# Optimization experiments

Hardware: AMD Instinct MI355X
Metric: run time of the kernel (lower is better)

## Reference

```python
import jax, jax.numpy as jnp
import numpy as np

HIDDEN = 100


def _mlp(x, w1, b1, w2, b2):
    # MLP(in, HIDDEN, output_size=out): Linear -> ReLU -> Linear
    return jnp.maximum(x @ w1 + b1, 0.0) @ w2 + b2


def _row_norm_mean(d):
    # mean_i sqrt(sum_j d_ij^2)  == torch.sqrt(einsum('ij,ij->i')).mean()
    return jnp.sqrt(jnp.einsum('ij,ij->i', d, d)).mean()


def _mismatch_1nn(mapped, target, idx):
    # torch_mapping_misclassified_1nn: cdist(mapped[idx], target), top-1 NN,
    # count non-integer distances at mismatched rows / len(idx).
    a = mapped[idx]                                     # [K, d]
    d2 = (jnp.sum(a * a, axis=1, keepdims=True)
          + jnp.sum(target * target, axis=1)[None, :]
          - 2.0 * a @ target.T)                         # [K, N]
    dist = jnp.sqrt(jnp.maximum(d2, 0.0))
    vals = jnp.min(dist, axis=1)                        # top-1 smallest value
    nn_inds = jnp.argmin(dist, axis=1)
    mismatch = (nn_inds != idx)
    count = (jnp.ceil(vals) - jnp.floor(vals)) * mismatch.astype(vals.dtype)
    return count.sum() / idx.shape[0]


def setup_inputs() -> dict:
    key = jax.random.key(0)
    ks = jax.random.split(key, 8)
    xN, yN, xd, yd, K = 25000, 25000, 100, 120, 8000
    s = 0.1
    return {
        'x_weight': jax.random.normal(ks[0], (xN, xd), jnp.float32) * s,
        'y_weight': jax.random.normal(ks[1], (yN, yd), jnp.float32) * s,
        'fx_w1': jax.random.normal(ks[2], (xd, HIDDEN), jnp.float32) * (1.0 / np.sqrt(xd)),
        'fx_b1': jnp.zeros((HIDDEN,), jnp.float32),
        'fx_w2': jax.random.normal(ks[3], (HIDDEN, yd), jnp.float32) * (1.0 / np.sqrt(HIDDEN)),
        'fx_b2': jnp.zeros((yd,), jnp.float32),
        'gy_w1': jax.random.normal(ks[4], (yd, HIDDEN), jnp.float32) * (1.0 / np.sqrt(yd)),
        'gy_b1': jnp.zeros((HIDDEN,), jnp.float32),
        'gy_w2': jax.random.normal(ks[5], (HIDDEN, xd), jnp.float32) * (1.0 / np.sqrt(HIDDEN)),
        'gy_b2': jnp.zeros((xd,), jnp.float32),
        'index_map': jax.random.randint(ks[6], (K, 2), 0, min(xN, yN), jnp.int64 if jax.config.jax_enable_x64 else jnp.int32),
    }


def reference(x_weight, y_weight, fx_w1, fx_b1, fx_w2, fx_b2,
              gy_w1, gy_b1, gy_w2, gy_b2, index_map):
    x_mapped = _mlp(x_weight, fx_w1, fx_b1, fx_w2, fx_b2)   # fx(x_emb)  [xN, yd]
    y_mapped = _mlp(y_weight, gy_w1, gy_b1, gy_w2, gy_b2)   # gy(y_emb)  [yN, xd]

    # cycle losses
    x_rt = _mlp(x_mapped, gy_w1, gy_b1, gy_w2, gy_b2)
    cycle_fx = _row_norm_mean(x_rt - x_weight)
    y_rt = _mlp(y_mapped, fx_w1, fx_b1, fx_w2, fx_b2)
    cycle_gy = _row_norm_mean(y_rt - y_weight)

    x_intersect = index_map[:, 0]
    y_intersect = index_map[:, 1]

    # supervised alignment losses
    sup_x = _row_norm_mean(x_mapped[x_intersect] - y_weight[y_intersect])
    sup_y = _row_norm_mean(y_mapped[y_intersect] - x_weight[x_intersect])

    # 1-NN mismatch losses (the cdist + top-1 hot spots)
    fx_mismatch = _mismatch_1nn(x_mapped, y_weight, x_intersect)
    gy_mismatch = _mismatch_1nn(y_mapped, x_weight, y_intersect)

    return cycle_fx + cycle_gy + sup_x + fx_mismatch + sup_y + gy_mismatch
```

## Files before the change

kernel.cpp:

```cpp
#include <hip/hip_runtime.h>
#include <hip/hip_bf16.h>
#include <math.h>

#define HIDDEN 100

typedef __attribute__((ext_vector_type(8))) short bf16x8;
typedef __attribute__((ext_vector_type(4))) float f32x4;

__device__ inline unsigned short f2bf(float v) {
    union { float f; unsigned u; } x; x.f = v;
    unsigned r = x.u + 0x7fff + ((x.u >> 16) & 1);
    return (unsigned short)(r >> 16);
}

constexpr int NPTS  = 25000;
constexpr int KPAIR = 8000;
constexpr int NC    = 28;
constexpr int CHUNK = 896;
constexpr int NPAD  = NC * CHUNK;
constexpr int HS    = 136;
constexpr int NB_SUP = 2000;
constexpr int GM     = (NPTS + 31) / 32;
constexpr int NB_MLP = 2 * GM;
constexpr int PREP_B = (2 * NPAD) / 16;

__global__ __launch_bounds__(256) void prep_kernel(
    const float* __restrict__ YW, float* __restrict__ tny, unsigned short* __restrict__ ybf,
    const float* __restrict__ XW, float* __restrict__ tnx, unsigned short* __restrict__ xbf,
    const float* __restrict__ W1, unsigned short* __restrict__ P1,
    const float* __restrict__ W2, unsigned short* __restrict__ P2,
    const float* __restrict__ W3, unsigned short* __restrict__ P3,
    const float* __restrict__ W4, unsigned short* __restrict__ P4,
    int N)
{
    const int ln = threadIdx.x & 63;
    if (blockIdx.x < PREP_B) {
        const int g0 = blockIdx.x * 16 + (threadIdx.x >> 6) * 4;
        #pragma unroll
        for (int i = 0; i < 4; i++) {
            const int gw = g0 + i;
            const int isY = (gw < NPAD);
            const int r = isY ? gw : gw - NPAD;
            const int D = isY ? 120 : 100;
            unsigned short* dst = (isY ? ybf : xbf) + (size_t)r * 128;
            if (r < N) {
                const float* src = (isY ? YW : XW) + (size_t)r * D;
                const float v0 = (ln < D) ? src[ln] : 0.f;
                const float v1 = (ln + 64 < D) ? src[ln + 64] : 0.f;
                float s = fmaf(v0, v0, v1 * v1);
                #pragma unroll
                for (int o = 1; o < 64; o <<= 1) s += __shfl_xor(s, o);
                if (ln == 0) (isY ? tny : tnx)[r] = s;
                dst[ln] = f2bf(v0);
                dst[ln + 64] = (ln == 63) ? f2bf(s) : f2bf(v1);
            } else {
                dst[ln] = 0;
                dst[ln + 64] = (ln == 63) ? f2bf(1e30f) : (unsigned short)0;
            }
        }
        return;
    }
    int b = (blockIdx.x - PREP_B) * 4 + (threadIdx.x >> 6);
    if (b >= 116) return;
    const float* W; unsigned short* P; int DK, DN, NT;
    if (b < 28)      {          W = W1; P = P1; DK = 100; DN = 100; NT = 7; }
    else if (b < 60) { b -= 28; W = W2; P = P2; DK = 100; DN = 120; NT = 8; }
    else if (b < 88) { b -= 60; W = W3; P = P3; DK = 120; DN = 100; NT = 7; }
    else             { b -= 88; W = W4; P = P4; DK = 100; DN = 100; NT = 7; }
    const int kt = b / NT, nt = b - kt * NT;
    const int n  = nt * 16 + (ln & 15);
    const int k0 = kt * 32 + (ln >> 4) * 8;
    unsigned short* dst = P + ((size_t)(kt * NT + nt) * 64 + ln) * 8;
    #pragma unroll
    for (int j = 0; j < 8; j++) {
        const int k = k0 + j;
        const float f = (k < DK && n < DN) ? W[k * DN + n] : 0.f;
        dst[j] = f2bf(f);
    }
}

template<int NT>
__device__ inline void run_stage(const bf16x8 af[4], const unsigned short* __restrict__ WP,
                                 int ln, f32x4 acc[NT])
{
    #pragma unroll
    for (int nt = 0; nt < NT; nt++) acc[nt] = (f32x4){0.f, 0.f, 0.f, 0.f};
    #pragma unroll
    for (int kt = 0; kt < 4; kt++) {
        #pragma unroll
        for (int nt = 0; nt < NT; nt++) {
            const bf16x8 wf = *reinterpret_cast<const bf16x8*>(WP + ((size_t)(kt * NT + nt) * 64 + ln) * 8);
            acc[nt] = __builtin_amdgcn_mfma_f32_16x16x32_bf16(af[kt], wf, acc[nt], 0, 0, 0);
        }
    }
}

template<int NT, int DN, bool RELU>
__device__ inline void pack_h(const f32x4 acc[NT], const float* __restrict__ B,
                              unsigned short* __restrict__ Hs, int col, int quad)
{
    #pragma unroll
    for (int nt = 0; nt < NT; nt++) {
        const int n = nt * 16 + col;
        const float b = (n < DN) ? B[n] : 0.f;
        #pragma unroll
        for (int r = 0; r < 4; r++) {
            float v = acc[nt][r] + b;
            if (RELU) v = fmaxf(v, 0.f);
            Hs[(quad * 4 + r) * HS + n] = f2bf(v);
        }
    }
}

template<int NT, int DN>
__device__ inline void store_pack(const f32x4 acc[NT], const float* __restrict__ B,
                                  float* __restrict__ Y, unsigned short* __restrict__ Hs,
                                  int rowbase, int col, int quad, int N)
{
    #pragma unroll
    for (int nt = 0; nt < NT; nt++) {
        const int n = nt * 16 + col;
        const float b = (n < DN) ? B[n] : 0.f;
        #pragma unroll
        for (int r = 0; r < 4; r++) {
            const float v = acc[nt][r] + b;
            const int row = rowbase + quad * 4 + r;
            if (n < DN && row < N) Y[(size_t)row * DN + n] = v;
            Hs[(quad * 4 + r) * HS + n] = f2bf(v);
        }
    }
}

__device__ inline void load_haf(const unsigned short* __restrict__ Hs, int col, int quad,
                                bf16x8 af[4])
{
    const unsigned short* p = Hs + col * HS + quad * 8;
    #pragma unroll
    for (int kt = 0; kt < 4; kt++)
        af[kt] = *reinterpret_cast<const bf16x8*>(p + kt * 32);
}

template<int NT, int DN>
__device__ inline float norm_stage(const f32x4 acc[NT], const float* __restrict__ B,
                                   const float* __restrict__ REF,
                                   int rowbase, int col, int quad, int N)
{
    float ra[4] = {0.f, 0.f, 0.f, 0.f};
    #pragma unroll
    for (int nt = 0; nt < NT; nt++) {
        const int n = nt * 16 + col;
        if (n < DN) {
            const float b = B[n];
            #pragma unroll
            for (int r = 0; r < 4; r++) {
                const int row = rowbase + quad * 4 + r;
                if (row < N) {
                    const float d = acc[nt][r] + b - REF[(size_t)row * DN + n];
                    ra[r] = fmaf(d, d, ra[r]);
                }
            }
        }
    }
    #pragma unroll
    for (int o = 1; o < 16; o <<= 1) {
        #pragma unroll
        for (int r = 0; r < 4; r++) ra[r] += __shfl_xor(ra[r], o);
    }
    float s = 0.f;
    if (col == 0) {
        #pragma unroll
        for (int r = 0; r < 4; r++)
            if (rowbase + quad * 4 + r < N) s += sqrtf(ra[r]);
    }
    return s;
}

template<int DIN, int DMID, int NT2, int NTF>
__device__ __forceinline__ void mlp_chain(
    int bid,
    const unsigned short* __restrict__ Xbf,
    const float* __restrict__ XREF,
    const unsigned short* __restrict__ WP1, const float* __restrict__ B1,
    const unsigned short* __restrict__ WP2, const float* __restrict__ B2,
    const unsigned short* __restrict__ WP3, const float* __restrict__ B3,
    const unsigned short* __restrict__ WP4, const float* __restrict__ B4,
    float* __restrict__ Y, float* __restrict__ part, int N,
    unsigned short (*H)[16 * HS], float* bred)
{
    const int tid = threadIdx.x;
    const int wv = tid >> 6, ln = tid & 63;
    const int col = ln & 15, quad = ln >> 4;
    const int rowbase = bid * 32 + wv * 16;

    {
        unsigned* Hz = reinterpret_cast<unsigned*>(H[wv]);
        for (int i = ln; i < 16 * HS / 2; i += 64) Hz[i] = 0u;
    }

    bf16x8 af[4];
    {
        const int r = min(rowbase + col, N - 1);
        const unsigned short* ap = Xbf + (size_t)r * 128 + quad * 8;
        #pragma unroll
        for (int kt = 0; kt < 4; kt++) af[kt] = *reinterpret_cast<const bf16x8*>(ap + kt * 32);
    }

    f32x4 accA[7];
    run_stage<7>(af, WP1, ln, accA);
    pack_h<7, HIDDEN, true>(accA, B1, H[wv], col, quad);
    load_haf(H[wv], col, quad, af);

    f32x4 accB[NT2];
    run_stage<NT2>(af, WP2, ln, accB);
    store_pack<NT2, DMID>(accB, B2, Y, H[wv], rowbase, col, quad, N);
    load_haf(H[wv], col, quad, af);

    run_stage<7>(af, WP3, ln, accA);
    pack_h<7, HIDDEN, true>(accA, B3, H[wv], col, quad);
    load_haf(H[wv], col, quad, af);

    f32x4 accC[NTF];
    run_stage<NTF>(af, WP4, ln, accC);
    const float s = norm_stage<NTF, DIN>(accC, B4, XREF, rowbase, col, quad, N);

    if (col == 0) bred[wv * 4 + quad] = s;
    __syncthreads();
    if (tid == 0) {
        float t = 0.f;
        #pragma unroll
        for (int i = 0; i < 8; i++) t += bred[i];
        part[bid] = t;
    }
}

__global__ __launch_bounds__(128) void mlp_both(
    const unsigned short* __restrict__ xbf, const float* __restrict__ xw,
    const unsigned short* __restrict__ ybf, const float* __restrict__ yw,
    const unsigned short* __restrict__ wp_fx1, const float* __restrict__ fx_b1,
    const unsigned short* __restrict__ wp_fx2, const float* __restrict__ fx_b2,
    const unsigned short* __restrict__ wp_gy1, const float* __restrict__ gy_b1,
    const unsigned short* __restrict__ wp_gy2, const float* __restrict__ gy_b2,
    float* __restrict__ xm, float* __restrict__ ym,
    float* __restrict__ part, int N)
{
    __shared__ unsigned short H[2][16 * HS];
    __shared__ float bred[8];
    if (blockIdx.x < GM) {
        mlp_chain<100, 120, 8, 7>(blockIdx.x, xbf, xw,
            wp_fx1, fx_b1, wp_fx2, fx_b2, wp_gy1, gy_b1, wp_gy2, gy_b2,
            xm, part, N, H, bred);
    } else {
        mlp_chain<120, 100, 7, 8>(blockIdx.x - GM, ybf, yw,
            wp_gy1, gy_b1, wp_gy2, gy_b2, wp_fx1, fx_b1, wp_fx2, fx_b2,
            ym, part + GM, N, H, bred);
    }
}

__global__ __launch_bounds__(256) void sup_gather(
    const float* __restrict__ xm, const float* __restrict__ ym,
    const float* __restrict__ xw, const float* __restrict__ yw,
    const int* __restrict__ im, int K, float* __restrict__ part,
    unsigned short* __restrict__ axf, unsigned short* __restrict__ ayf)
{
    const int gw = (int)((blockIdx.x * 256 + threadIdx.x) >> 6);
    const int ln = threadIdx.x & 63;
    const int wv = threadIdx.x >> 6;
    float cnt = 0.f;
    if (gw < K) {
        const int xi = im[2 * gw], yi = im[2 * gw + 1];
        const float* a = xm + (size_t)xi * 120;
        const float* b = yw + (size_t)yi * 120;
        const float a0 = a[ln];
        const float a1 = (ln + 64 < 120) ? a[ln + 64] : 0.f;
        float s1 = 0.f;
        { const float d0 = a0 - b[ln]; s1 = d0 * d0; }
        if (ln + 64 < 120) { const float d1 = a1 - b[ln + 64]; s1 = fmaf(d1, d1, s1); }
        unsigned short* pax = axf + (size_t)gw * 128;
        pax[ln] = f2bf(-2.f * a0);
        pax[ln + 64] = (ln == 63) ? f2bf(1.f) : ((ln + 64 < 120) ? f2bf(-2.f * a1) : (unsigned short)0);

        const float* c = ym + (size_t)yi * 100;
        const float* e = xw + (size_t)xi * 100;
        const float c0 = c[ln];
        const float c1 = (ln + 64 < 100) ? c[ln + 64] : 0.f;
        float s2 = 0.f;
        { const float d0 = c0 - e[ln]; s2 = d0 * d0; }
        if (ln + 64 < 100) { const float d1 = c1 - e[ln + 64]; s2 = fmaf(d1, d1, s2); }
        unsigned short* pay = ayf + (size_t)gw * 128;
        pay[ln] = f2bf(-2.f * c0);
        pay[ln + 64] = (ln == 63) ? f2bf(1.f) : ((ln + 64 < 100) ? f2bf(-2.f * c1) : (unsigned short)0);

        #pragma unroll
        for (int o = 32; o > 0; o >>= 1) { s1 += __shfl_down(s1, o); s2 += __shfl_down(s2, o); }
        if (ln == 0) cnt = sqrtf(s1) + sqrtf(s2);
    }
    __shared__ float wsum[4];
    if (ln == 0) wsum[wv] = cnt;
    __syncthreads();
    if (threadIdx.x == 0)
        part[blockIdx.x] = wsum[0] + wsum[1] + wsum[2] + wsum[3];
}

__device__ inline void stage32(const unsigned short* __restrict__ T, int jbase,
                               unsigned char* dst0, int wv, int ln)
{
    #pragma unroll
    for (int h = 0; h < 2; h++) {
        const int c = h * 256 + wv * 64 + ln;
        const int r = c >> 4;
        const int gc = (c & 15) ^ (r & 15);
        const unsigned short* g = T + ((size_t)(jbase + r) << 7) + gc * 8;
        unsigned char* l = dst0 + h * 4096 + wv * 1024;
        __builtin_amdgcn_global_load_lds(
            (const __attribute__((address_space(1))) void*)g,
            (__attribute__((address_space(3))) void*)l, 16, 0, 0);
    }
}

__global__ __launch_bounds__(256, 3) void nn_mfma(
    const unsigned short* __restrict__ A0, const unsigned short* __restrict__ T0,
    float* __restrict__ pm0, int* __restrict__ pi0,
    const unsigned short* __restrict__ A1, const unsigned short* __restrict__ T1,
    float* __restrict__ pm1, int* __restrict__ pi1,
    int K)
{
    __shared__ __align__(16) unsigned char smem[32768];
    float (*rm)[64][17] = reinterpret_cast<float(*)[64][17]>(smem);

    const unsigned short* A = blockIdx.z ? A1 : A0;
    const unsigned short* T = blockIdx.z ? T1 : T0;
    float* pmin = blockIdx.z ? pm1 : pm0;
    int*   pidx = blockIdx.z ? pi1 : pi0;

    const int tid = threadIdx.x;
    const int wv = tid >> 6, ln = tid & 63;
    const int col = ln & 15, quad = ln >> 4;
    const int k0 = blockIdx.x * 256;
    const int jstart = blockIdx.y * CHUNK;
    constexpr int NSTEPS = CHUNK / 64;

    bf16x8 afrag[4][4];
    #pragma unroll
    for (int t = 0; t < 4; t++) {
        const int ar = min(k0 + wv * 64 + t * 16 + col, K - 1);
        const unsigned short* ab = A + (size_t)ar * 128 + quad * 8;
        #pragma unroll
        for (int s = 0; s < 4; s++)
            afrag[t][s] = *reinterpret_cast<const bf16x8*>(ab + s * 32);
    }

    float m[4][4];
    #pragma unroll
    for (int t = 0; t < 4; t++)
        #pragma unroll
        for (int r = 0; r < 4; r++) m[t][r] = __builtin_inff();

    stage32(T, jstart,      smem,        wv, ln);
    stage32(T, jstart + 32, smem + 8192, wv, ln);
    __syncthreads();

    for (int ti = 0; ti < NSTEPS; ti++) {
        const int cur = ti & 1;
        if (ti + 1 < NSTEPS) {
            const int jn = jstart + (ti + 1) * 64;
            stage32(T, jn,      smem + (cur ^ 1) * 16384,        wv, ln);
            stage32(T, jn + 32, smem + (cur ^ 1) * 16384 + 8192, wv, ln);
        }

        #pragma unroll
        for (int h = 0; h < 2; h++) {
            const unsigned short* base = (const unsigned short*)(smem + cur * 16384 + h * 8192);
            const unsigned lowbase = (unsigned)((jstart + ti * 64 + h * 32) >> 4);
            #pragma unroll
            for (int sub = 0; sub < 2; sub++) {
                bf16x8 bfr[4];
                const int rr = sub * 16 + col;
                #pragma unroll
                for (int s = 0; s < 4; s++) {
                    const int ch = rr * 16 + ((quad + s * 4) ^ col);
                    bfr[s] = *reinterpret_cast<const bf16x8*>(base + ch * 8);
                }
                const unsigned low = lowbase + sub;
                #pragma unroll
                for (int t = 0; t < 4; t++) {
                    f32x4 acc = {0.f, 0.f, 0.f, 0.f};
                    #pragma unroll
                    for (int s = 0; s < 4; s++)
                        acc = __builtin_amdgcn_mfma_f32_16x16x32_bf16(afrag[t][s], bfr[s], acc, 0, 0, 0);
                    #pragma unroll
                    for (int r = 0; r < 4; r++) {
                        const unsigned u = (__float_as_uint(acc[r]) & 0xFFFFF800u) | low;
                        m[t][r] = fminf(m[t][r], __uint_as_float(u));
                    }
                }
            }
        }
        __syncthreads();
    }

    #pragma unroll
    for (int t = 0; t < 4; t++)
        #pragma unroll
        for (int r = 0; r < 4; r++)
            rm[wv][t * 16 + quad * 4 + r][col] = m[t][r];
    __syncthreads();

    const int k = k0 + tid;
    if (k < K) {
        const int w = tid >> 6, rr = tid & 63;
        float best = rm[w][rr][0];
        int bc = 0;
        #pragma unroll
        for (int c = 1; c < 16; c++) {
            const float v = rm[w][rr][c];
            if (v < best) { best = v; bc = c; }
        }
        const int j = (int)(((__float_as_uint(best) & 0x7FFu) << 4) | (unsigned)bc);
        pmin[(size_t)k * NC + blockIdx.y] = best;
        pidx[(size_t)k * NC + blockIdx.y] = j;
    }
}

__global__ __launch_bounds__(256) void finish_all(
    const int* __restrict__ im,
    const float* __restrict__ pm0, const int* __restrict__ pi0,
    const float* __restrict__ pm1, const int* __restrict__ pi1,
    const float* __restrict__ part_sup, const float* __restrict__ part_mlp,
    int K, float* __restrict__ out, float inv_k, float inv_n)
{
    const int gid = blockIdx.x * 256 + threadIdx.x;
    const int stride = gridDim.x * 256;
    float local = 0.f;

    for (int p = gid; p < 2 * K; p += stride) {
        const int dir = (p >= K);
        const int kk = dir ? p - K : p;
        const float* pm = dir ? pm1 : pm0;
        const int*   pi = dir ? pi1 : pi0;
        float best = __builtin_inff();
        int bi = 0x7fffffff;
        #pragma unroll
        for (int c = 0; c < NC; c++) {
            const float v = pm[(size_t)kk * NC + c];
            const int  ii = pi[(size_t)kk * NC + c];
            if (v < best || (v == best && ii < bi)) { best = v; bi = ii; }
        }
        if (bi != im[2 * kk + dir]) local += inv_k;
    }
    for (int i = gid; i < NB_SUP; i += stride) local += part_sup[i] * inv_k;
    for (int i = gid; i < NB_MLP; i += stride) local += part_mlp[i] * inv_n;

    #pragma unroll
    for (int o = 32; o > 0; o >>= 1) local += __shfl_down(local, o);
    __shared__ float wsum[4];
    if ((threadIdx.x & 63) == 0) wsum[threadIdx.x >> 6] = local;
    __syncthreads();
    if (threadIdx.x == 0) {
        const float t = wsum[0] + wsum[1] + wsum[2] + wsum[3];
        if (t != 0.f) atomicAdd(out, t);
    }
}

extern "C" void kernel_launch(void* const* d_in, const int* in_sizes, int n_in,
                              void* d_out, int out_size, void* d_ws, size_t ws_size,
                              hipStream_t stream)
{
    const float* xw    = (const float*)d_in[0];
    const float* yw    = (const float*)d_in[1];
    const float* fx_w1 = (const float*)d_in[2];
    const float* fx_b1 = (const float*)d_in[3];
    const float* fx_w2 = (const float*)d_in[4];
    const float* fx_b2 = (const float*)d_in[5];
    const float* gy_w1 = (const float*)d_in[6];
    const float* gy_b1 = (const float*)d_in[7];
    const float* gy_w2 = (const float*)d_in[8];
    const float* gy_b2 = (const float*)d_in[9];
    const int*   imap  = (const int*)d_in[10];
    float* out = (float*)d_out;
    float* ws  = (float*)d_ws;

    constexpr int N = NPTS, K = KPAIR;

    float* xm      = ws;
    float* ym      = xm + (size_t)N * 120;
    float* tn_y    = ym + (size_t)N * 100;
    float* tn_x    = tn_y + N;
    float* pmin_fx = tn_x + N;
    int*   pidx_fx = (int*)(pmin_fx + (size_t)K * NC);
    float* pmin_gy = (float*)(pidx_fx + (size_t)K * NC);
    int*   pidx_gy = (int*)(pmin_gy + (size_t)K * NC);
    unsigned short* ybf = (unsigned short*)(pidx_gy + (size_t)K * NC);
    unsigned short* xbf = ybf + (size_t)NPAD * 128;
    unsigned short* axf = xbf + (size_t)NPAD * 128;
    unsigned short* ayf = axf + (size_t)K * 128;
    unsigned short* wp_fx1 = ayf + (size_t)K * 128;
    unsigned short* wp_fx2 = wp_fx1 + 28 * 512;
    unsigned short* wp_gy1 = wp_fx2 + 32 * 512;
    unsigned short* wp_gy2 = wp_gy1 + 28 * 512;
    float* part_sup = (float*)(wp_gy2 + 28 * 512);
    float* part_mlp = part_sup + NB_SUP;

    hipMemsetAsync(d_out, 0, sizeof(float), stream);

    prep_kernel<<<PREP_B + 29, 256, 0, stream>>>(
        yw, tn_y, ybf, xw, tn_x, xbf,
        fx_w1, wp_fx1, fx_w2, wp_fx2, gy_w1, wp_gy1, gy_w2, wp_gy2, N);

    mlp_both<<<2 * GM, 128, 0, stream>>>(
        xbf, xw, ybf, yw,
        wp_fx1, fx_b1, wp_fx2, fx_b2, wp_gy1, gy_b1, wp_gy2, gy_b2,
        xm, ym, part_mlp, N);

    sup_gather<<<NB_SUP, 256, 0, stream>>>(xm, ym, xw, yw, imap, K, part_sup, axf, ayf);

    dim3 g1((K + 255) / 256, NC, 2);
    nn_mfma<<<g1, 256, 0, stream>>>(axf, ybf, pmin_fx, pidx_fx,
                                    ayf, xbf, pmin_gy, pidx_gy, K);

    finish_all<<<64, 256, 0, stream>>>(
        imap, pmin_fx, pidx_fx, pmin_gy, pidx_gy, part_sup, part_mlp,
        K, out, 1.f / K, 1.f / N);
}
```

Before: 217.9 us.

## Fold embedding bf16 conversion into MLP kernel and load fp32 inputs directly

```diff
diff --git a/kernel.cpp b/kernel.cpp
--- a/kernel.cpp
+++ b/kernel.cpp
@@ -22,45 +22,16 @@
 constexpr int NB_SUP = 2000;
 constexpr int GM     = (NPTS + 31) / 32;
 constexpr int NB_MLP = 2 * GM;
-constexpr int PREP_B = (2 * NPAD) / 16;
-
-__global__ __launch_bounds__(256) void prep_kernel(
-    const float* __restrict__ YW, float* __restrict__ tny, unsigned short* __restrict__ ybf,
-    const float* __restrict__ XW, float* __restrict__ tnx, unsigned short* __restrict__ xbf,
+constexpr int PREP_B8 = (2 * NPAD) / 8;
+
+__global__ __launch_bounds__(256) void w_prep(
     const float* __restrict__ W1, unsigned short* __restrict__ P1,
     const float* __restrict__ W2, unsigned short* __restrict__ P2,
     const float* __restrict__ W3, unsigned short* __restrict__ P3,
-    const float* __restrict__ W4, unsigned short* __restrict__ P4,
-    int N)
+    const float* __restrict__ W4, unsigned short* __restrict__ P4)
 {
     const int ln = threadIdx.x & 63;
-    if (blockIdx.x < PREP_B) {
-        const int g0 = blockIdx.x * 16 + (threadIdx.x >> 6) * 4;
-        #pragma unroll
-        for (int i = 0; i < 4; i++) {
-            const int gw = g0 + i;
-            const int isY = (gw < NPAD);
-            const int r = isY ? gw : gw - NPAD;
-            const int D = isY ? 120 : 100;
-            unsigned short* dst = (isY ? ybf : xbf) + (size_t)r * 128;
-            if (r < N) {
-                const float* src = (isY ? YW : XW) + (size_t)r * D;
-                const float v0 = (ln < D) ? src[ln] : 0.f;
-                const float v1 = (ln + 64 < D) ? src[ln + 64] : 0.f;
-                float s = fmaf(v0, v0, v1 * v1);
-                #pragma unroll
-                for (int o = 1; o < 64; o <<= 1) s += __shfl_xor(s, o);
-                if (ln == 0) (isY ? tny : tnx)[r] = s;
-                dst[ln] = f2bf(v0);
-                dst[ln + 64] = (ln == 63) ? f2bf(s) : f2bf(v1);
-            } else {
-                dst[ln] = 0;
-                dst[ln + 64] = (ln == 63) ? f2bf(1e30f) : (unsigned short)0;
-            }
-        }
-        return;
-    }
-    int b = (blockIdx.x - PREP_B) * 4 + (threadIdx.x >> 6);
+    int b = blockIdx.x * 4 + (threadIdx.x >> 6);
     if (b >= 116) return;
     const float* W; unsigned short* P; int DK, DN, NT;
     if (b < 28)      {          W = W1; P = P1; DK = 100; DN = 100; NT = 7; }
@@ -138,6 +109,38 @@
     #pragma unroll
     for (int kt = 0; kt < 4; kt++)
         af[kt] = *reinterpret_cast<const bf16x8*>(p + kt * 32);
+}
+
+template<int DIN>
+__device__ inline void load_a_direct(const float* __restrict__ X, int r, int quad,
+                                     bf16x8 af[4])
+{
+    const float* ap = X + (size_t)r * DIN;
+    #pragma unroll
+    for (int kt = 0; kt < 4; kt++) {
+        const int base = kt * 32 + quad * 8;
+        float4 v0, v1;
+        if (DIN == 100) {
+            if (base == 96) {
+                v0 = *reinterpret_cast<const float4*>(ap + 96);
+                v1 = make_float4(0.f, 0.f, 0.f, 0.f);
+            } else {
+                const int b = (base < 92) ? base : 92;
+                v0 = *reinterpret_cast<const float4*>(ap + b);
+                v1 = *reinterpret_cast<const float4*>(ap + b + 4);
+            }
+        } else {
+            const int b = (base < 112) ? base : 112;
+            v0 = *reinterpret_cast<const float4*>(ap + b);
+            v1 = *reinterpret_cast<const float4*>(ap + b + 4);
+        }
+        bf16x8 f;
+        f[0] = (short)f2bf(v0.x); f[1] = (short)f2bf(v0.y);
+        f[2] = (short)f2bf(v0.z); f[3] = (short)f2bf(v0.w);
+        f[4] = (short)f2bf(v1.x); f[5] = (short)f2bf(v1.y);
+        f[6] = (short)f2bf(v1.z); f[7] = (short)f2bf(v1.w);
+        af[kt] = f;
+    }
 }
 
 template<int NT, int DN>
@@ -178,7 +181,6 @@
 template<int DIN, int DMID, int NT2, int NTF>
 __device__ __forceinline__ void mlp_chain(
     int bid,
-    const unsigned short* __restrict__ Xbf,
     const float* __restrict__ XREF,
     const unsigned short* __restrict__ WP1, const float* __restrict__ B1,
     const unsigned short* __restrict__ WP2, const float* __restrict__ B2,
@@ -198,12 +200,7 @@
     }
 
     bf16x8 af[4];
-    {
-        const int r = min(rowbase + col, N - 1);
-        const unsigned short* ap = Xbf + (size_t)r * 128 + quad * 8;
-        #pragma unroll
-        for (int kt = 0; kt < 4; kt++) af[kt] = *reinterpret_cast<const bf16x8*>(ap + kt * 32);
-    }
+    load_a_direct<DIN>(XREF, min(rowbase + col, N - 1), quad, af);
 
     f32x4 accA[7];
     run_stage<7>(af, WP1, ln, accA);
@@ -233,9 +230,9 @@
     }
 }
 
-__global__ __launch_bounds__(128) void mlp_both(
-    const unsigned short* __restrict__ xbf, const float* __restrict__ xw,
-    const unsigned short* __restrict__ ybf, const float* __restrict__ yw,
+__global__ __launch_bounds__(128) void mlp_prep(
+    const float* __restrict__ xw, const float* __restrict__ yw,
+    unsigned short* __restrict__ ybf, unsigned short* __restrict__ xbf,
     const unsigned short* __restrict__ wp_fx1, const float* __restrict__ fx_b1,
     const unsigned short* __restrict__ wp_fx2, const float* __restrict__ fx_b2,
     const unsigned short* __restrict__ wp_gy1, const float* __restrict__ gy_b1,
@@ -245,14 +242,42 @@
 {
     __shared__ unsigned short H[2][16 * HS];
     __shared__ float bred[8];
+
     if (blockIdx.x < GM) {
-        mlp_chain<100, 120, 8, 7>(blockIdx.x, xbf, xw,
+        mlp_chain<100, 120, 8, 7>(blockIdx.x, xw,
             wp_fx1, fx_b1, wp_fx2, fx_b2, wp_gy1, gy_b1, wp_gy2, gy_b2,
             xm, part, N, H, bred);
-    } else {
-        mlp_chain<120, 100, 7, 8>(blockIdx.x - GM, ybf, yw,
+        return;
+    }
+    if (blockIdx.x < 2 * GM) {
+        mlp_chain<120, 100, 7, 8>(blockIdx.x - GM, yw,
             wp_gy1, gy_b1, wp_gy2, gy_b2, wp_fx1, fx_b1, wp_fx2, fx_b2,
             ym, part + GM, N, H, bred);
+        return;
+    }
+
+    const int bid = blockIdx.x - 2 * GM;
+    const int wv = threadIdx.x >> 6, ln = threadIdx.x & 63;
+    #pragma unroll
+    for (int i = 0; i < 4; i++) {
+        const int gw = bid * 8 + wv * 4 + i;
+        const int isY = (gw < NPAD);
+        const int r = isY ? gw : gw - NPAD;
+        const int D = isY ? 120 : 100;
+        unsigned short* dst = (isY ? ybf : xbf) + (size_t)r * 128;
+        if (r < N) {
+            const float* src = (isY ? yw : xw) + (size_t)r * D;
+            const float v0 = (ln < D) ? src[ln] : 0.f;
+            const float v1 = (ln + 64 < D) ? src[ln + 64] : 0.f;
+            float s = fmaf(v0, v0, v1 * v1);
+            #pragma unroll
+            for (int o = 1; o < 64; o <<= 1) s += __shfl_xor(s, o);
+            dst[ln] = f2bf(v0);
+            dst[ln + 64] = (ln == 63) ? f2bf(s) : f2bf(v1);
+        } else {
+            dst[ln] = 0;
+            dst[ln + 64] = (ln == 63) ? f2bf(1e30f) : (unsigned short)0;
+        }
     }
 }
 
@@ -483,9 +508,7 @@
 
     float* xm      = ws;
     float* ym      = xm + (size_t)N * 120;
-    float* tn_y    = ym + (size_t)N * 100;
-    float* tn_x    = tn_y + N;
-    float* pmin_fx = tn_x + N;
+    float* pmin_fx = ym + (size_t)N * 100;
     int*   pidx_fx = (int*)(pmin_fx + (size_t)K * NC);
     float* pmin_gy = (float*)(pidx_fx + (size_t)K * NC);
     int*   pidx_gy = (int*)(pmin_gy + (size_t)K * NC);
@@ -502,12 +525,11 @@
 
     hipMemsetAsync(d_out, 0, sizeof(float), stream);
 
-    prep_kernel<<<PREP_B + 29, 256, 0, stream>>>(
-        yw, tn_y, ybf, xw, tn_x, xbf,
-        fx_w1, wp_fx1, fx_w2, wp_fx2, gy_w1, wp_gy1, gy_w2, wp_gy2, N);
-
-    mlp_both<<<2 * GM, 128, 0, stream>>>(
-        xbf, xw, ybf, yw,
+    w_prep<<<29, 256, 0, stream>>>(fx_w1, wp_fx1, fx_w2, wp_fx2,
+                                   gy_w1, wp_gy1, gy_w2, wp_gy2);
+
+    mlp_prep<<<2 * GM + PREP_B8, 128, 0, stream>>>(
+        xw, yw, ybf, xbf,
         wp_fx1, fx_b1, wp_fx2, fx_b2, wp_gy1, gy_b1, wp_gy2, gy_b2,
         xm, ym, part_mlp, N);
 
```

After: 226.3 us. +3.9%, slower.
